# Kernel optimization log

Hardware: AMD Instinct MI355X
Metric: run time of the kernel (lower is better)

The kernel has to match this reference:

```python
import jax, jax.numpy as jnp
import numpy as np
import math

E, K = 8, 4
IN, OUT = 768, 768
B, S = 16, 512

def _nearest_factors(n):
    r = int(math.sqrt(n))
    while n % r != 0:
        r -= 1
    r = max(r, 1)
    return r, n // r

D1, D2 = _nearest_factors(IN)      # 24, 32
DO1, DO2 = _nearest_factors(OUT)   # 24, 32

def _cv_squared(v):
    v = v.astype(jnp.float32)
    return jnp.var(v, ddof=1) / (jnp.mean(v) ** 2 + 1e-10)

def setup_inputs() -> dict:
    key = jax.random.key(0)
    ks = jax.random.split(key, 8)
    eye = lambda d: jnp.broadcast_to(jnp.eye(d, dtype=jnp.float32), (E, d, d))
    return {
        "x": jax.random.normal(ks[0], (B, S, IN), jnp.float32),
        "w_gate": 0.02 * jax.random.normal(ks[1], (IN, E), jnp.float32),
        "weight": 0.02 * jax.random.normal(ks[2], (E, OUT, IN), jnp.float32),
        "res_weight": 0.02 * jax.random.normal(ks[3], (OUT, IN), jnp.float32),
        "curve1_in": eye(D1) + 0.01 * jax.random.normal(ks[4], (E, D1, D1), jnp.float32),
        "curve2_in": eye(D2) + 0.01 * jax.random.normal(ks[5], (E, D2, D2), jnp.float32),
        "curve1_out": eye(DO1) + 0.01 * jax.random.normal(ks[6], (E, DO1, DO1), jnp.float32),
        "curve2_out": eye(DO2) + 0.01 * jax.random.normal(ks[7], (E, DO2, DO2), jnp.float32),
    }

def reference(x, w_gate, weight, res_weight, curve1_in, curve2_in, curve1_out, curve2_out):
    b = x.shape[0]
    # ---- noisy_top_k_gating (eval mode: clean logits, no noise) ----
    xm = x.mean(-2)                         # [B, IN]
    logits = xm @ w_gate                    # [B, E]
    top_vals, top_idx = jax.lax.top_k(logits, min(K + 1, E))
    tk_vals = top_vals[:, :K]
    tk_idx = top_idx[:, :K]
    tk_gates = jax.nn.softmax(tk_vals, axis=1)
    gates = jnp.zeros_like(logits).at[jnp.arange(b)[:, None], tk_idx].set(tk_gates)
    load = (gates > 0).sum(0)               # eval: gates_to_load
    importance = gates.sum(0)
    loss = 0.01 * (_cv_squared(importance) + _cv_squared(load))
    # ---- curve-factor expert weight composition (k*2 >= n_experts branch) ----
    rtw = (weight - res_weight).reshape(E, DO1, DO2, D1, D2)
    rtw = jnp.einsum('bij,bjklm->biklm', curve1_out, rtw)
    rtw = jnp.einsum('bik,bjklm->bjilm', curve2_out, rtw)
    rtw = jnp.einsum('bil,bjklm->bjkim', curve1_in, rtw)
    rtw = jnp.einsum('bim,bjklm->bjkli', curve2_in, rtw)
    rtw = rtw.reshape(E, OUT, IN)
    # dropout p=0.1 is identity in eval mode
    expert_weights = res_weight + 0.9 * jnp.sum(rtw[None] * gates[:, :, None, None], axis=1)  # [B, OUT, IN]
    y = jnp.einsum('bsj,bkj->bsk', x, expert_weights)  # [B, S, OUT]
    return y, loss
```

## Files before the change

kernel.cpp:

```cpp
#include <hip/hip_runtime.h>
#include <hip/hip_bf16.h>

typedef unsigned short u16;
typedef __attribute__((ext_vector_type(8))) short bf16x8;
typedef __attribute__((ext_vector_type(4))) float f32x4;

#define NE 8
#define NTOPK 4
#define NIN 768
#define NOUT 768
#define NB 16
#define NS 512
#define YSZ (NB * NS * NOUT)
#define EWN (NOUT * NIN)

#define OFF_PART  0u
#define OFF_GATES 3145728u
#define OFF_XBF   3146240u
#define OFF_WD    15729152u
#define OFF_T1T   25166336u
#define OFF_RTW   34603520u
#define OFF_EW    44040704u

#define PRE_BAR(N) asm volatile("s_waitcnt vmcnt(" #N ")\n\ts_barrier" ::: "memory")
#define POST_BAR() asm volatile("s_waitcnt lgkmcnt(0)\n\ts_barrier" ::: "memory")

__device__ __forceinline__ u16 f2bf(float f) {
  union { float f; unsigned u; } v; v.f = f;
  unsigned r = v.u + 0x7fffu + ((v.u >> 16) & 1u);
  return (u16)(r >> 16);
}
__device__ __forceinline__ float bf2f(u16 h) {
  union { unsigned u; float f; } v; v.u = ((unsigned)h) << 16;
  return v.f;
}
__device__ __forceinline__ unsigned cvt2(float a, float b) {
  unsigned r;
  asm("v_cvt_pk_bf16_f32 %0, %1, %2" : "=v"(r) : "v"(a), "v"(b));
  return r;
}

__device__ __forceinline__ void gload16(const void* g, void* l) {
  __builtin_amdgcn_global_load_lds(
      (const __attribute__((address_space(1))) unsigned int*)g,
      (__attribute__((address_space(3))) unsigned int*)l, 16, 0, 0);
}

__device__ __forceinline__ void storeC(float* p, float v) { *p = v; }
__device__ __forceinline__ void storeC(u16* p, float v) { *p = f2bf(v); }

__global__ __launch_bounds__(256) void k_xm_wd(const float* __restrict__ x,
                                               float* __restrict__ part,
                                               u16* __restrict__ xbf,
                                               const float* __restrict__ w,
                                               const float* __restrict__ res,
                                               u16* __restrict__ Wd) {
  int bid = blockIdx.x;
  if (bid < 1024) {
    int t = threadIdx.x;
    if (t < 192) {
      int b = bid >> 6;
      int sc = bid & 63;
      int c = t * 4;
      float a0 = 0.f, a1 = 0.f, a2 = 0.f, a3 = 0.f;
      int s0 = sc * 8;
#pragma unroll
      for (int r = 0; r < 8; ++r) {
        size_t ro = ((size_t)(b * NS + s0 + r)) * NIN;
        float4 v = *(const float4*)(x + ro + c);
        a0 += v.x; a1 += v.y; a2 += v.z; a3 += v.w;
        ushort4 o;
        o.x = f2bf(v.x); o.y = f2bf(v.y); o.z = f2bf(v.z); o.w = f2bf(v.w);
        *(ushort4*)(xbf + ro + c) = o;
      }
      float4 pv; pv.x = a0; pv.y = a1; pv.z = a2; pv.w = a3;
      *(float4*)(part + (size_t)(b * 64 + sc) * NIN + c) = pv;
    }
  } else {
    int b2 = bid - 1024;
    int e = b2 / 288;
    int blk = b2 % 288;
    size_t base = (size_t)blk * 2048 + threadIdx.x * 8;
    float4 wa = *(const float4*)(w + (size_t)e * EWN + base);
    float4 wb = *(const float4*)(w + (size_t)e * EWN + base + 4);
    float4 ra = *(const float4*)(res + base);
    float4 rb = *(const float4*)(res + base + 4);
    bf16x8 o;
    o[0] = (short)f2bf(wa.x - ra.x); o[1] = (short)f2bf(wa.y - ra.y);
    o[2] = (short)f2bf(wa.z - ra.z); o[3] = (short)f2bf(wa.w - ra.w);
    o[4] = (short)f2bf(wb.x - rb.x); o[5] = (short)f2bf(wb.y - rb.y);
    o[6] = (short)f2bf(wb.z - rb.z); o[7] = (short)f2bf(wb.w - rb.w);
    *(bf16x8*)(Wd + (size_t)e * EWN + base) = o;
  }
}

__global__ __launch_bounds__(256) void gemm_kron(const float* __restrict__ c1,
                                                 const float* __restrict__ c2,
                                                 const u16* __restrict__ B,
                                                 u16* __restrict__ C,
                                                 const float* __restrict__ part,
                                                 const float* __restrict__ w_gate,
                                                 float* __restrict__ gates_out) {
  __shared__ u16 lB[4][128 * 32];
  __shared__ float red[4 * NE];
  const int tid = threadIdx.x;

  if (blockIdx.x >= 576) {
    if (!gates_out) return;
    int b = blockIdx.x - 576;
    float p[NE] = {0.f, 0.f, 0.f, 0.f, 0.f, 0.f, 0.f, 0.f};
    for (int i = tid; i < NIN; i += 256) {
      float s = 0.f;
#pragma unroll
      for (int sc = 0; sc < 64; ++sc) s += part[(size_t)(b * 64 + sc) * NIN + i];
      float xmv = s * (1.0f / (float)NS);
#pragma unroll
      for (int e = 0; e < NE; ++e) p[e] += xmv * w_gate[i * NE + e];
    }
#pragma unroll
    for (int e = 0; e < NE; ++e) {
      float v = p[e];
      for (int off = 32; off; off >>= 1) v += __shfl_down(v, off);
      if ((tid & 63) == 0) red[(tid >> 6) * NE + e] = v;
    }
    __syncthreads();
    if (tid == 0) {
      float v[NE]; bool used[NE];
      for (int e = 0; e < NE; ++e) {
        v[e] = red[e] + red[NE + e] + red[2 * NE + e] + red[3 * NE + e];
        used[e] = false;
      }
      int idxs[NTOPK]; float vals[NTOPK];
      for (int t = 0; t < NTOPK; ++t) {
        int best = 0; float bv = -3.4e38f;
        for (int e = 0; e < NE; ++e)
          if (!used[e] && v[e] > bv) { bv = v[e]; best = e; }
        used[best] = true; idxs[t] = best; vals[t] = bv;
      }
      float m = vals[0];
      float ex[NTOPK]; float se = 0.f;
      for (int t = 0; t < NTOPK; ++t) { ex[t] = expf(vals[t] - m); se += ex[t]; }
      float g[NE];
      for (int e = 0; e < NE; ++e) g[e] = 0.f;
      for (int t = 0; t < NTOPK; ++t) g[idxs[t]] = ex[t] / se;
      for (int e = 0; e < NE; ++e) gates_out[b * NE + e] = g[e];
    }
    return;
  }

  const int lane = tid & 63;
  const int w = tid >> 6;
  const int wr = w >> 1, wc = w & 1;
  const int fr = lane & 15;
  const int kq = lane >> 4;

  const int swz = (blockIdx.x & 7) * 72 + (blockIdx.x >> 3);
  const int mb = swz % 12;
  const int nb = (swz / 12) % 6;
  const int e = swz / 72;

  const int m0 = mb * 64, n0 = nb * 128;
  const u16* Bb = B + (size_t)e * EWN;
  const float* c1b = c1 + e * 24 * 24;
  const float* c2b = c2 + e * 32 * 32;

  const int r1a = (m0 >> 5) + wr;
  float c2r[2][8];
  {
    const float* p0 = c2b + fr * 32 + kq * 8;
    const float* p1 = c2b + (16 + fr) * 32 + kq * 8;
#pragma unroll
    for (int j = 0; j < 8; ++j) { c2r[0][j] = p0[j]; c2r[1][j] = p1[j]; }
  }

  const int ob1 = (w * 2) * 1024 + lane * 16;
  const int ob2 = ob1 + 1024;
  const int rowB1 = ob1 >> 6, colB1 = ob1 & 63;
  const int rowB2 = ob2 >> 6, colB2 = ob2 & 63;

  auto STAGE = [&](int t) {
    int s = t & 3;
    int k0 = t * 32;
    gload16((const char*)Bb + ((size_t)(n0 + rowB1) * NIN + k0) * 2 + colB1,
            (char*)&lB[s][0] + ob1);
    gload16((const char*)Bb + ((size_t)(n0 + rowB2) * NIN + k0) * 2 + colB2,
            (char*)&lB[s][0] + ob2);
  };

  f32x4 acc[2][4] = {};

  auto COMPUTE = [&](int t) {
    int s = t & 3;
    const float ca = c1b[r1a * 24 + t];
    bf16x8 aF[2], bF[4];
#pragma unroll
    for (int m = 0; m < 2; ++m) {
      union { unsigned u[4]; bf16x8 v; } pk;
      pk.u[0] = cvt2(ca * c2r[m][0], ca * c2r[m][1]);
      pk.u[1] = cvt2(ca * c2r[m][2], ca * c2r[m][3]);
      pk.u[2] = cvt2(ca * c2r[m][4], ca * c2r[m][5]);
      pk.u[3] = cvt2(ca * c2r[m][6], ca * c2r[m][7]);
      aF[m] = pk.v;
    }
#pragma unroll
    for (int n = 0; n < 4; ++n)
      bF[n] = *(const bf16x8*)&lB[s][(wc * 64 + n * 16 + fr) * 32 + kq * 8];
#pragma unroll
    for (int m = 0; m < 2; ++m)
#pragma unroll
      for (int n = 0; n < 4; ++n)
        acc[m][n] = __builtin_amdgcn_mfma_f32_16x16x32_bf16(aF[m], bF[n], acc[m][n], 0, 0, 0);
  };

  STAGE(0); STAGE(1); STAGE(2); STAGE(3);
  for (int i = 0; i < 10; ++i) {
    PRE_BAR(4);
    COMPUTE(2 * i); COMPUTE(2 * i + 1);
    POST_BAR();
    STAGE(2 * i + 4); STAGE(2 * i + 5);
  }
  PRE_BAR(4);  COMPUTE(20); COMPUTE(21);  POST_BAR();
  PRE_BAR(0);  COMPUTE(22); COMPUTE(23);

  u16* Cb = C + (size_t)e * EWN;
#pragma unroll
  for (int m = 0; m < 2; ++m) {
    int rb = m0 + wr * 32 + m * 16 + kq * 4;
#pragma unroll
    for (int n = 0; n < 4; ++n) {
      int col = n0 + wc * 64 + n * 16 + fr;
#pragma unroll
      for (int r = 0; r < 4; ++r)
        storeC(&Cb[(size_t)(rb + r) * NIN + col], acc[m][n][r]);
    }
  }
}

__global__ __launch_bounds__(256) void gemm_main(const u16* __restrict__ A,
                                                 const u16* __restrict__ Bw,
                                                 float* __restrict__ C) {
  __shared__ u16 lA[4][64 * 32];
  __shared__ u16 lB[4][128 * 32];
  const int tid = threadIdx.x;
  const int lane = tid & 63;
  const int w = tid >> 6;
  const int wr = w >> 1, wc = w & 1;
  const int fr = lane & 15;
  const int kq = lane >> 4;

  const int swz = (blockIdx.x & 7) * 96 + (blockIdx.x >> 3);
  const int mb = swz % 8;
  const int nb = (swz / 8) % 6;
  const int b = swz / 48;

  const int m0 = mb * 64, n0 = nb * 128;
  const u16* Ab = A + (size_t)b * NS * NIN;
  const u16* Bb = Bw + (size_t)b * EWN;

  const int obA = tid * 16;
  const int rowA = obA >> 6, colA = obA & 63;
  const int obB1 = (w * 2) * 1024 + lane * 16;
  const int obB2 = obB1 + 1024;
  const int rowB1 = obB1 >> 6, colB1 = obB1 & 63;
  const int rowB2 = obB2 >> 6, colB2 = obB2 & 63;

  auto STAGE = [&](int t) {
    int s = t & 3;
    int k0 = t * 32;
    gload16((const char*)Ab + ((size_t)(m0 + rowA) * NIN + k0) * 2 + colA,
            (char*)&lA[s][0] + obA);
    gload16((const char*)Bb + ((size_t)(n0 + rowB1) * NIN + k0) * 2 + colB1,
            (char*)&lB[s][0] + obB1);
    gload16((const char*)Bb + ((size_t)(n0 + rowB2) * NIN + k0) * 2 + colB2,
            (char*)&lB[s][0] + obB2);
  };

  f32x4 acc[2][4] = {};

  auto COMPUTE = [&](int t) {
    int s = t & 3;
    bf16x8 aF[2], bF[4];
#pragma unroll
    for (int m = 0; m < 2; ++m)
      aF[m] = *(const bf16x8*)&lA[s][(wr * 32 + m * 16 + fr) * 32 + kq * 8];
#pragma unroll
    for (int n = 0; n < 4; ++n)
      bF[n] = *(const bf16x8*)&lB[s][(wc * 64 + n * 16 + fr) * 32 + kq * 8];
#pragma unroll
    for (int m = 0; m < 2; ++m)
#pragma unroll
      for (int n = 0; n < 4; ++n)
        acc[m][n] = __builtin_amdgcn_mfma_f32_16x16x32_bf16(aF[m], bF[n], acc[m][n], 0, 0, 0);
  };

  STAGE(0); STAGE(1); STAGE(2); STAGE(3);
  for (int i = 0; i < 10; ++i) {
    PRE_BAR(6);
    COMPUTE(2 * i); COMPUTE(2 * i + 1);
    POST_BAR();
    STAGE(2 * i + 4); STAGE(2 * i + 5);
  }
  PRE_BAR(6);  COMPUTE(20); COMPUTE(21);  POST_BAR();
  PRE_BAR(0);  COMPUTE(22); COMPUTE(23);

  float* Cb = C + (size_t)b * NS * NOUT;
#pragma unroll
  for (int m = 0; m < 2; ++m) {
    int rb = m0 + wr * 32 + m * 16 + kq * 4;
#pragma unroll
    for (int n = 0; n < 4; ++n) {
      int col = n0 + wc * 64 + n * 16 + fr;
#pragma unroll
      for (int r = 0; r < 4; ++r)
        Cb[(size_t)(rb + r) * NOUT + col] = acc[m][n][r];
    }
  }
}

__global__ __launch_bounds__(256) void k_combine(const u16* __restrict__ rtwb,
                                                 const float* __restrict__ res,
                                                 const float* __restrict__ g,
                                                 u16* __restrict__ ew,
                                                 float* __restrict__ loss_out) {
  __shared__ float gs[NB * NE];
  int tid = threadIdx.x;
  if (tid < NB * NE) gs[tid] = 0.9f * g[tid];
  __syncthreads();
  if (blockIdx.x == 0 && tid == 0) {
    float imp[NE], ld[NE];
    for (int e = 0; e < NE; ++e) {
      float si = 0.f, sl = 0.f;
      for (int b = 0; b < NB; ++b) {
        float gg = g[b * NE + e];
        si += gg; sl += (gg > 0.f) ? 1.f : 0.f;
      }
      imp[e] = si; ld[e] = sl;
    }
    float loss = 0.f;
    for (int which = 0; which < 2; ++which) {
      const float* a = which ? ld : imp;
      float mean = 0.f;
      for (int e = 0; e < NE; ++e) mean += a[e];
      mean *= (1.0f / NE);
      float var = 0.f;
      for (int e = 0; e < NE; ++e) { float d = a[e] - mean; var += d * d; }
      var *= (1.0f / (NE - 1));
      loss += var / (mean * mean + 1e-10f);
    }
    loss_out[0] = 0.01f * loss;
  }
  size_t base = ((size_t)blockIdx.x * 256 + tid) * 8;
  float rv[NE][8];
#pragma unroll
  for (int e = 0; e < NE; ++e) {
    bf16x8 v = *(const bf16x8*)(rtwb + (size_t)e * EWN + base);
#pragma unroll
    for (int j = 0; j < 8; ++j) rv[e][j] = bf2f((u16)v[j]);
  }
  float r8[8];
  {
    float4 ra = *(const float4*)(res + base);
    float4 rb = *(const float4*)(res + base + 4);
    r8[0] = ra.x; r8[1] = ra.y; r8[2] = ra.z; r8[3] = ra.w;
    r8[4] = rb.x; r8[5] = rb.y; r8[6] = rb.z; r8[7] = rb.w;
  }
  for (int b = 0; b < NB; ++b) {
    float a[8];
#pragma unroll
    for (int j = 0; j < 8; ++j) a[j] = r8[j];
#pragma unroll
    for (int e = 0; e < NE; ++e) {
      float gg = gs[b * NE + e];
#pragma unroll
      for (int j = 0; j < 8; ++j) a[j] += gg * rv[e][j];
    }
    bf16x8 o;
#pragma unroll
    for (int j = 0; j < 8; ++j) o[j] = (short)f2bf(a[j]);
    *(bf16x8*)(ew + (size_t)b * EWN + base) = o;
  }
}

extern "C" void kernel_launch(void* const* d_in, const int* in_sizes, int n_in,
                              void* d_out, int out_size, void* d_ws, size_t ws_size,
                              hipStream_t stream) {
  const float* x = (const float*)d_in[0];
  const float* w_gate = (const float*)d_in[1];
  const float* weight = (const float*)d_in[2];
  const float* res_w = (const float*)d_in[3];
  const float* c1i = (const float*)d_in[4];
  const float* c2i = (const float*)d_in[5];
  const float* c1o = (const float*)d_in[6];
  const float* c2o = (const float*)d_in[7];

  char* ws = (char*)d_ws;
  float* part = (float*)(ws + OFF_PART);
  float* gates = (float*)(ws + OFF_GATES);
  u16* xbf = (u16*)(ws + OFF_XBF);
  u16* Wd = (u16*)(ws + OFF_WD);
  u16* T1t = (u16*)(ws + OFF_T1T);
  u16* rtwb = (u16*)(ws + OFF_RTW);
  u16* ew = (u16*)(ws + OFF_EW);

  float* y = (float*)d_out;
  float* loss = y + YSZ;

  k_xm_wd<<<dim3(3328), 256, 0, stream>>>(x, part, xbf, weight, res_w, Wd);
  gemm_kron<<<dim3(592), 256, 0, stream>>>(c1i, c2i, Wd, T1t, part, w_gate, gates);
  gemm_kron<<<dim3(576), 256, 0, stream>>>(c1o, c2o, T1t, rtwb, nullptr, nullptr, nullptr);
  k_combine<<<dim3(288), 256, 0, stream>>>(rtwb, res_w, gates, ew, loss);
  gemm_main<<<dim3(768), 256, 0, stream>>>(xbf, ew, y);
}
```

Measured before the change: 76.94 us.

## Fuse five kernel stages into one cooperative persistent kernel with grid syncs

Merges the five launches (x mean/bf16 cast plus weight delta, two Kronecker GEMMs with gating, combine, main GEMM) into a single cooperative kernel of 768 blocks that separates the stages with grid.sync. If the occupancy check or cooperative launch fails, it falls back to the original five-launch sequence. The aim is to remove per-launch overhead and the gaps between kernels. In exchange, each phase is limited to 768 resident blocks, shared memory is sized for the largest phase, and every grid barrier adds its own cost.

```diff
diff --git a/kernel.cpp b/kernel.cpp
--- a/kernel.cpp
+++ b/kernel.cpp
@@ -1,5 +1,8 @@
 #include <hip/hip_runtime.h>
 #include <hip/hip_bf16.h>
+#include <hip/hip_cooperative_groups.h>
+
+namespace cg = cooperative_groups;
 
 typedef unsigned short u16;
 typedef __attribute__((ext_vector_type(8))) short bf16x8;
@@ -13,6 +16,7 @@
 #define NS 512
 #define YSZ (NB * NS * NOUT)
 #define EWN (NOUT * NIN)
+#define NBLK 768
 
 #define OFF_PART  0u
 #define OFF_GATES 3145728u
@@ -39,28 +43,24 @@
   asm("v_cvt_pk_bf16_f32 %0, %1, %2" : "=v"(r) : "v"(a), "v"(b));
   return r;
 }
-
 __device__ __forceinline__ void gload16(const void* g, void* l) {
   __builtin_amdgcn_global_load_lds(
       (const __attribute__((address_space(1))) unsigned int*)g,
       (__attribute__((address_space(3))) unsigned int*)l, 16, 0, 0);
 }
-
 __device__ __forceinline__ void storeC(float* p, float v) { *p = v; }
 __device__ __forceinline__ void storeC(u16* p, float v) { *p = f2bf(v); }
 
-__global__ __launch_bounds__(256) void k_xm_wd(const float* __restrict__ x,
-                                               float* __restrict__ part,
-                                               u16* __restrict__ xbf,
-                                               const float* __restrict__ w,
-                                               const float* __restrict__ res,
-                                               u16* __restrict__ Wd) {
-  int bid = blockIdx.x;
-  if (bid < 1024) {
+__device__ __forceinline__ void body_xmwd(int u, const float* __restrict__ x,
+                                          float* __restrict__ part, u16* __restrict__ xbf,
+                                          const float* __restrict__ w,
+                                          const float* __restrict__ res,
+                                          u16* __restrict__ Wd) {
+  if (u < 1024) {
     int t = threadIdx.x;
     if (t < 192) {
-      int b = bid >> 6;
-      int sc = bid & 63;
+      int b = u >> 6;
+      int sc = u & 63;
       int c = t * 4;
       float a0 = 0.f, a1 = 0.f, a2 = 0.f, a3 = 0.f;
       int s0 = sc * 8;
@@ -77,7 +77,7 @@
       *(float4*)(part + (size_t)(b * 64 + sc) * NIN + c) = pv;
     }
   } else {
-    int b2 = bid - 1024;
+    int b2 = u - 1024;
     int e = b2 / 288;
     int blk = b2 % 288;
     size_t base = (size_t)blk * 2048 + threadIdx.x * 8;
@@ -94,76 +94,69 @@
   }
 }
 
-__global__ __launch_bounds__(256) void gemm_kron(const float* __restrict__ c1,
-                                                 const float* __restrict__ c2,
-                                                 const u16* __restrict__ B,
-                                                 u16* __restrict__ C,
-                                                 const float* __restrict__ part,
-                                                 const float* __restrict__ w_gate,
-                                                 float* __restrict__ gates_out) {
-  __shared__ u16 lB[4][128 * 32];
-  __shared__ float red[4 * NE];
+__device__ __forceinline__ void body_logits(int b, float* red,
+                                            const float* __restrict__ part,
+                                            const float* __restrict__ w_gate,
+                                            float* __restrict__ gates_out) {
+  int tid = threadIdx.x;
+  float p[NE] = {0.f, 0.f, 0.f, 0.f, 0.f, 0.f, 0.f, 0.f};
+  for (int i = tid; i < NIN; i += 256) {
+    float s = 0.f;
+#pragma unroll
+    for (int sc = 0; sc < 64; ++sc) s += part[(size_t)(b * 64 + sc) * NIN + i];
+    float xmv = s * (1.0f / (float)NS);
+#pragma unroll
+    for (int e = 0; e < NE; ++e) p[e] += xmv * w_gate[i * NE + e];
+  }
+#pragma unroll
+  for (int e = 0; e < NE; ++e) {
+    float v = p[e];
+    for (int off = 32; off; off >>= 1) v += __shfl_down(v, off);
+    if ((tid & 63) == 0) red[(tid >> 6) * NE + e] = v;
+  }
+  __syncthreads();
+  if (tid == 0) {
+    float v[NE]; bool used[NE];
+    for (int e = 0; e < NE; ++e) {
+      v[e] = red[e] + red[NE + e] + red[2 * NE + e] + red[3 * NE + e];
+      used[e] = false;
+    }
+    int idxs[NTOPK]; float vals[NTOPK];
+    for (int t = 0; t < NTOPK; ++t) {
+      int best = 0; float bv = -3.4e38f;
+      for (int e = 0; e < NE; ++e)
+        if (!used[e] && v[e] > bv) { bv = v[e]; best = e; }
+      used[best] = true; idxs[t] = best; vals[t] = bv;
+    }
+    float m = vals[0];
+    float ex[NTOPK]; float se = 0.f;
+    for (int t = 0; t < NTOPK; ++t) { ex[t] = expf(vals[t] - m); se += ex[t]; }
+    float g[NE];
+    for (int e = 0; e < NE; ++e) g[e] = 0.f;
+    for (int t = 0; t < NTOPK; ++t) g[idxs[t]] = ex[t] / se;
+    for (int e = 0; e < NE; ++e) gates_out[b * NE + e] = g[e];
+  }
+}
+
+__device__ __forceinline__ void body_kron(int bid, u16* lb,
+                                          const float* __restrict__ c1,
+                                          const float* __restrict__ c2,
+                                          const u16* __restrict__ B,
+                                          u16* __restrict__ C) {
   const int tid = threadIdx.x;
-
-  if (blockIdx.x >= 576) {
-    if (!gates_out) return;
-    int b = blockIdx.x - 576;
-    float p[NE] = {0.f, 0.f, 0.f, 0.f, 0.f, 0.f, 0.f, 0.f};
-    for (int i = tid; i < NIN; i += 256) {
-      float s = 0.f;
-#pragma unroll
-      for (int sc = 0; sc < 64; ++sc) s += part[(size_t)(b * 64 + sc) * NIN + i];
-      float xmv = s * (1.0f / (float)NS);
-#pragma unroll
-      for (int e = 0; e < NE; ++e) p[e] += xmv * w_gate[i * NE + e];
-    }
-#pragma unroll
-    for (int e = 0; e < NE; ++e) {
-      float v = p[e];
-      for (int off = 32; off; off >>= 1) v += __shfl_down(v, off);
-      if ((tid & 63) == 0) red[(tid >> 6) * NE + e] = v;
-    }
-    __syncthreads();
-    if (tid == 0) {
-      float v[NE]; bool used[NE];
-      for (int e = 0; e < NE; ++e) {
-        v[e] = red[e] + red[NE + e] + red[2 * NE + e] + red[3 * NE + e];
-        used[e] = false;
-      }
-      int idxs[NTOPK]; float vals[NTOPK];
-      for (int t = 0; t < NTOPK; ++t) {
-        int best = 0; float bv = -3.4e38f;
-        for (int e = 0; e < NE; ++e)
-          if (!used[e] && v[e] > bv) { bv = v[e]; best = e; }
-        used[best] = true; idxs[t] = best; vals[t] = bv;
-      }
-      float m = vals[0];
-      float ex[NTOPK]; float se = 0.f;
-      for (int t = 0; t < NTOPK; ++t) { ex[t] = expf(vals[t] - m); se += ex[t]; }
-      float g[NE];
-      for (int e = 0; e < NE; ++e) g[e] = 0.f;
-      for (int t = 0; t < NTOPK; ++t) g[idxs[t]] = ex[t] / se;
-      for (int e = 0; e < NE; ++e) gates_out[b * NE + e] = g[e];
-    }
-    return;
-  }
-
   const int lane = tid & 63;
   const int w = tid >> 6;
   const int wr = w >> 1, wc = w & 1;
   const int fr = lane & 15;
   const int kq = lane >> 4;
-
-  const int swz = (blockIdx.x & 7) * 72 + (blockIdx.x >> 3);
+  const int swz = (bid & 7) * 72 + (bid >> 3);
   const int mb = swz % 12;
   const int nb = (swz / 12) % 6;
   const int e = swz / 72;
-
   const int m0 = mb * 64, n0 = nb * 128;
   const u16* Bb = B + (size_t)e * EWN;
   const float* c1b = c1 + e * 24 * 24;
   const float* c2b = c2 + e * 32 * 32;
-
   const int r1a = (m0 >> 5) + wr;
   float c2r[2][8];
   {
@@ -172,7 +165,6 @@
 #pragma unroll
     for (int j = 0; j < 8; ++j) { c2r[0][j] = p0[j]; c2r[1][j] = p1[j]; }
   }
-
   const int ob1 = (w * 2) * 1024 + lane * 16;
   const int ob2 = ob1 + 1024;
   const int rowB1 = ob1 >> 6, colB1 = ob1 & 63;
@@ -182,13 +174,11 @@
     int s = t & 3;
     int k0 = t * 32;
     gload16((const char*)Bb + ((size_t)(n0 + rowB1) * NIN + k0) * 2 + colB1,
-            (char*)&lB[s][0] + ob1);
+            (char*)(lb + s * 4096) + ob1);
     gload16((const char*)Bb + ((size_t)(n0 + rowB2) * NIN + k0) * 2 + colB2,
-            (char*)&lB[s][0] + ob2);
+            (char*)(lb + s * 4096) + ob2);
   };
-
   f32x4 acc[2][4] = {};
-
   auto COMPUTE = [&](int t) {
     int s = t & 3;
     const float ca = c1b[r1a * 24 + t];
@@ -204,7 +194,7 @@
     }
 #pragma unroll
     for (int n = 0; n < 4; ++n)
-      bF[n] = *(const bf16x8*)&lB[s][(wc * 64 + n * 16 + fr) * 32 + kq * 8];
+      bF[n] = *(const bf16x8*)(lb + (size_t)s * 4096 + (wc * 64 + n * 16 + fr) * 32 + kq * 8);
 #pragma unroll
     for (int m = 0; m < 2; ++m)
 #pragma unroll
@@ -231,102 +221,21 @@
       int col = n0 + wc * 64 + n * 16 + fr;
 #pragma unroll
       for (int r = 0; r < 4; ++r)
-        storeC(&Cb[(size_t)(rb + r) * NIN + col], acc[m][n][r]);
-    }
-  }
-}
-
-__global__ __launch_bounds__(256) void gemm_main(const u16* __restrict__ A,
-                                                 const u16* __restrict__ Bw,
-                                                 float* __restrict__ C) {
-  __shared__ u16 lA[4][64 * 32];
-  __shared__ u16 lB[4][128 * 32];
-  const int tid = threadIdx.x;
-  const int lane = tid & 63;
-  const int w = tid >> 6;
-  const int wr = w >> 1, wc = w & 1;
-  const int fr = lane & 15;
-  const int kq = lane >> 4;
-
-  const int swz = (blockIdx.x & 7) * 96 + (blockIdx.x >> 3);
-  const int mb = swz % 8;
-  const int nb = (swz / 8) % 6;
-  const int b = swz / 48;
-
-  const int m0 = mb * 64, n0 = nb * 128;
-  const u16* Ab = A + (size_t)b * NS * NIN;
-  const u16* Bb = Bw + (size_t)b * EWN;
-
-  const int obA = tid * 16;
-  const int rowA = obA >> 6, colA = obA & 63;
-  const int obB1 = (w * 2) * 1024 + lane * 16;
-  const int obB2 = obB1 + 1024;
-  const int rowB1 = obB1 >> 6, colB1 = obB1 & 63;
-  const int rowB2 = obB2 >> 6, colB2 = obB2 & 63;
-
-  auto STAGE = [&](int t) {
-    int s = t & 3;
-    int k0 = t * 32;
-    gload16((const char*)Ab + ((size_t)(m0 + rowA) * NIN + k0) * 2 + colA,
-            (char*)&lA[s][0] + obA);
-    gload16((const char*)Bb + ((size_t)(n0 + rowB1) * NIN + k0) * 2 + colB1,
-            (char*)&lB[s][0] + obB1);
-    gload16((const char*)Bb + ((size_t)(n0 + rowB2) * NIN + k0) * 2 + colB2,
-            (char*)&lB[s][0] + obB2);
-  };
-
-  f32x4 acc[2][4] = {};
-
-  auto COMPUTE = [&](int t) {
-    int s = t & 3;
-    bf16x8 aF[2], bF[4];
-#pragma unroll
-    for (int m = 0; m < 2; ++m)
-      aF[m] = *(const bf16x8*)&lA[s][(wr * 32 + m * 16 + fr) * 32 + kq * 8];
-#pragma unroll
-    for (int n = 0; n < 4; ++n)
-      bF[n] = *(const bf16x8*)&lB[s][(wc * 64 + n * 16 + fr) * 32 + kq * 8];
-#pragma unroll
-    for (int m = 0; m < 2; ++m)
-#pragma unroll
-      for (int n = 0; n < 4; ++n)
-        acc[m][n] = __builtin_amdgcn_mfma_f32_16x16x32_bf16(aF[m], bF[n], acc[m][n], 0, 0, 0);
-  };
-
-  STAGE(0); STAGE(1); STAGE(2); STAGE(3);
-  for (int i = 0; i < 10; ++i) {
-    PRE_BAR(6);
-    COMPUTE(2 * i); COMPUTE(2 * i + 1);
-    POST_BAR();
-    STAGE(2 * i + 4); STAGE(2 * i + 5);
-  }
-  PRE_BAR(6);  COMPUTE(20); COMPUTE(21);  POST_BAR();
-  PRE_BAR(0);  COMPUTE(22); COMPUTE(23);
-
-  float* Cb = C + (size_t)b * NS * NOUT;
-#pragma unroll
-  for (int m = 0; m < 2; ++m) {
-    int rb = m0 + wr * 32 + m * 16 + kq * 4;
-#pragma unroll
-    for (int n = 0; n < 4; ++n) {
-      int col = n0 + wc * 64 + n * 16 + fr;
-#pragma unroll
-      for (int r = 0; r < 4; ++r)
-        Cb[(size_t)(rb + r) * NOUT + col] = acc[m][n][r];
-    }
-  }
-}
-
-__global__ __launch_bounds__(256) void k_combine(const u16* __restrict__ rtwb,
-                                                 const float* __restrict__ res,
-                                                 const float* __restrict__ g,
-                                                 u16* __restrict__ ew,
-                                                 float* __restrict__ loss_out) {
-  __shared__ float gs[NB * NE];
+        storeC(Cb + (size_t)(rb + r) * NIN + col, acc[m][n][r]);
+    }
+  }
+}
+
+__device__ __forceinline__ void body_combine(int bid, float* gsh,
+                                             const u16* __restrict__ rtwb,
+                                             const float* __restrict__ res,
+                                             const float* __restrict__ g,
+                                             u16* __restrict__ ew,
+                                             float* __restrict__ loss_out) {
   int tid = threadIdx.x;
-  if (tid < NB * NE) gs[tid] = 0.9f * g[tid];
+  if (tid < NB * NE) gsh[tid] = 0.9f * g[tid];
   __syncthreads();
-  if (blockIdx.x == 0 && tid == 0) {
+  if (bid == 0 && tid == 0) {
     float imp[NE], ld[NE];
     for (int e = 0; e < NE; ++e) {
       float si = 0.f, sl = 0.f;
@@ -349,7 +258,7 @@
     }
     loss_out[0] = 0.01f * loss;
   }
-  size_t base = ((size_t)blockIdx.x * 256 + tid) * 8;
+  size_t base = ((size_t)bid * 256 + tid) * 8;
   float rv[NE][8];
 #pragma unroll
   for (int e = 0; e < NE; ++e) {
@@ -370,7 +279,7 @@
     for (int j = 0; j < 8; ++j) a[j] = r8[j];
 #pragma unroll
     for (int e = 0; e < NE; ++e) {
-      float gg = gs[b * NE + e];
+      float gg = gsh[b * NE + e];
 #pragma unroll
       for (int j = 0; j < 8; ++j) a[j] += gg * rv[e][j];
     }
@@ -379,6 +288,143 @@
     for (int j = 0; j < 8; ++j) o[j] = (short)f2bf(a[j]);
     *(bf16x8*)(ew + (size_t)b * EWN + base) = o;
   }
+}
+
+__device__ __forceinline__ void body_main(int bid, u16* la, u16* lb,
+                                          const u16* __restrict__ A,
+                                          const u16* __restrict__ Bw,
+                                          float* __restrict__ C) {
+  const int tid = threadIdx.x;
+  const int lane = tid & 63;
+  const int w = tid >> 6;
+  const int wr = w >> 1, wc = w & 1;
+  const int fr = lane & 15;
+  const int kq = lane >> 4;
+  const int swz = (bid & 7) * 96 + (bid >> 3);
+  const int mb = swz % 8;
+  const int nb = (swz / 8) % 6;
+  const int b = swz / 48;
+  const int m0 = mb * 64, n0 = nb * 128;
+  const u16* Ab = A + (size_t)b * NS * NIN;
+  const u16* Bb = Bw + (size_t)b * EWN;
+  const int obA = tid * 16;
+  const int rowA = obA >> 6, colA = obA & 63;
+  const int obB1 = (w * 2) * 1024 + lane * 16;
+  const int obB2 = obB1 + 1024;
+  const int rowB1 = obB1 >> 6, colB1 = obB1 & 63;
+  const int rowB2 = obB2 >> 6, colB2 = obB2 & 63;
+
+  auto STAGE = [&](int t) {
+    int s = t & 3;
+    int k0 = t * 32;
+    gload16((const char*)Ab + ((size_t)(m0 + rowA) * NIN + k0) * 2 + colA,
+            (char*)(la + s * 2048) + obA);
+    gload16((const char*)Bb + ((size_t)(n0 + rowB1) * NIN + k0) * 2 + colB1,
+            (char*)(lb + s * 4096) + obB1);
+    gload16((const char*)Bb + ((size_t)(n0 + rowB2) * NIN + k0) * 2 + colB2,
+            (char*)(lb + s * 4096) + obB2);
+  };
+  f32x4 acc[2][4] = {};
+  auto COMPUTE = [&](int t) {
+    int s = t & 3;
+    bf16x8 aF[2], bF[4];
+#pragma unroll
+    for (int m = 0; m < 2; ++m)
+      aF[m] = *(const bf16x8*)(la + (size_t)s * 2048 + (wr * 32 + m * 16 + fr) * 32 + kq * 8);
+#pragma unroll
+    for (int n = 0; n < 4; ++n)
+      bF[n] = *(const bf16x8*)(lb + (size_t)s * 4096 + (wc * 64 + n * 16 + fr) * 32 + kq * 8);
+#pragma unroll
+    for (int m = 0; m < 2; ++m)
+#pragma unroll
+      for (int n = 0; n < 4; ++n)
+        acc[m][n] = __builtin_amdgcn_mfma_f32_16x16x32_bf16(aF[m], bF[n], acc[m][n], 0, 0, 0);
+  };
+
+  STAGE(0); STAGE(1); STAGE(2); STAGE(3);
+  for (int i = 0; i < 10; ++i) {
+    PRE_BAR(6);
+    COMPUTE(2 * i); COMPUTE(2 * i + 1);
+    POST_BAR();
+    STAGE(2 * i + 4); STAGE(2 * i + 5);
+  }
+  PRE_BAR(6);  COMPUTE(20); COMPUTE(21);  POST_BAR();
+  PRE_BAR(0);  COMPUTE(22); COMPUTE(23);
+
+  float* Cb = C + (size_t)b * NS * NOUT;
+#pragma unroll
+  for (int m = 0; m < 2; ++m) {
+    int rb = m0 + wr * 32 + m * 16 + kq * 4;
+#pragma unroll
+    for (int n = 0; n < 4; ++n) {
+      int col = n0 + wc * 64 + n * 16 + fr;
+#pragma unroll
+      for (int r = 0; r < 4; ++r)
+        Cb[(size_t)(rb + r) * NOUT + col] = acc[m][n][r];
+    }
+  }
+}
+
+__global__ __launch_bounds__(256, 3) void mega(const float* __restrict__ x,
+                                               const float* __restrict__ w_gate,
+                                               const float* __restrict__ weight,
+                                               const float* __restrict__ res_w,
+                                               const float* __restrict__ c1i,
+                                               const float* __restrict__ c2i,
+                                               const float* __restrict__ c1o,
+                                               const float* __restrict__ c2o,
+                                               float* part, float* gates,
+                                               u16* xbf, u16* Wd, u16* T1t, u16* rtwb,
+                                               u16* ew, float* y, float* lossp) {
+  __shared__ __attribute__((aligned(128))) u16 lA0[4 * 64 * 32];
+  __shared__ __attribute__((aligned(128))) u16 lB0[4 * 128 * 32];
+  cg::grid_group grid = cg::this_grid();
+  const int bid = blockIdx.x;
+
+  for (int u = bid; u < 3328; u += NBLK)
+    body_xmwd(u, x, part, xbf, weight, res_w, Wd);
+  grid.sync();
+
+  if (bid < 576)       body_kron(bid, lB0, c1i, c2i, Wd, T1t);
+  else if (bid < 592)  body_logits(bid - 576, (float*)lA0, part, w_gate, gates);
+  grid.sync();
+
+  if (bid < 576)       body_kron(bid, lB0, c1o, c2o, T1t, rtwb);
+  grid.sync();
+
+  if (bid < 288)       body_combine(bid, (float*)lA0, rtwb, res_w, gates, ew, lossp);
+  grid.sync();
+
+  body_main(bid, lA0, lB0, xbf, ew, y);
+}
+
+__global__ __launch_bounds__(256) void k_p0(const float* x, float* part, u16* xbf,
+                                            const float* w, const float* res, u16* Wd) {
+  body_xmwd(blockIdx.x, x, part, xbf, w, res, Wd);
+}
+__global__ __launch_bounds__(256) void k_p1(const float* c1, const float* c2,
+                                            const u16* B, u16* C,
+                                            const float* part, const float* w_gate,
+                                            float* gates) {
+  __shared__ __attribute__((aligned(128))) u16 lB[4 * 128 * 32];
+  __shared__ float red[4 * NE];
+  if (blockIdx.x < 576) body_kron(blockIdx.x, lB, c1, c2, B, C);
+  else                  body_logits(blockIdx.x - 576, red, part, w_gate, gates);
+}
+__global__ __launch_bounds__(256) void k_p2(const float* c1, const float* c2,
+                                            const u16* B, u16* C) {
+  __shared__ __attribute__((aligned(128))) u16 lB[4 * 128 * 32];
+  body_kron(blockIdx.x, lB, c1, c2, B, C);
+}
+__global__ __launch_bounds__(256) void k_p3(const u16* rtwb, const float* res,
+                                            const float* g, u16* ew, float* loss) {
+  __shared__ float gsh[NB * NE];
+  body_combine(blockIdx.x, gsh, rtwb, res, g, ew, loss);
+}
+__global__ __launch_bounds__(256) void k_p4(const u16* A, const u16* Bw, float* C) {
+  __shared__ __attribute__((aligned(128))) u16 lA[4 * 64 * 32];
+  __shared__ __attribute__((aligned(128))) u16 lB[4 * 128 * 32];
+  body_main(blockIdx.x, lA, lB, A, Bw, C);
 }
 
 extern "C" void kernel_launch(void* const* d_in, const int* in_sizes, int n_in,
@@ -405,9 +451,23 @@
   float* y = (float*)d_out;
   float* loss = y + YSZ;
 
-  k_xm_wd<<<dim3(3328), 256, 0, stream>>>(x, part, xbf, weight, res_w, Wd);
-  gemm_kron<<<dim3(592), 256, 0, stream>>>(c1i, c2i, Wd, T1t, part, w_gate, gates);
-  gemm_kron<<<dim3(576), 256, 0, stream>>>(c1o, c2o, T1t, rtwb, nullptr, nullptr, nullptr);
-  k_combine<<<dim3(288), 256, 0, stream>>>(rtwb, res_w, gates, ew, loss);
-  gemm_main<<<dim3(768), 256, 0, stream>>>(xbf, ew, y);
-}
+  int occ = 0;
+  bool coop =
+      (hipOccupancyMaxActiveBlocksPerMultiprocessor(&occ, mega, 256, 0) == hipSuccess) &&
+      occ >= 3;
+  if (coop) {
+    void* args[] = {(void*)&x, (void*)&w_gate, (void*)&weight, (void*)&res_w,
+                    (void*)&c1i, (void*)&c2i, (void*)&c1o, (void*)&c2o,
+                    (void*)&part, (void*)&gates, (void*)&xbf, (void*)&Wd,
+                    (void*)&T1t, (void*)&rtwb, (void*)&ew, (void*)&y, (void*)&loss};
+    coop = (hipLaunchCooperativeKernel((const void*)mega, dim3(NBLK), dim3(256),
+                                       args, 0, stream) == hipSuccess);
+  }
+  if (!coop) {
+    k_p0<<<dim3(3328), 256, 0, stream>>>(x, part, xbf, weight, res_w, Wd);
+    k_p1<<<dim3(592), 256, 0, stream>>>(c1i, c2i, Wd, T1t, part, w_gate, gates);
+    k_p2<<<dim3(576), 256, 0, stream>>>(c1o, c2o, T1t, rtwb);
+    k_p3<<<dim3(288), 256, 0, stream>>>(rtwb, res_w, gates, ew, loss);
+    k_p4<<<dim3(768), 256, 0, stream>>>(xbf, ew, y);
+  }
+}
```

After: 77.65 us. No clear change (+0.9%).
